# Optimization experiments

Hardware: AMD Instinct MI355X
Metric: run time of the kernel (lower is better)

The kernel has to match this reference:

```python
import jax, jax.numpy as jnp
import numpy as np

D_EMB = 256


def setup_inputs() -> dict:
    key = jax.random.key(0)
    ks = jax.random.split(key, 7)
    B, S, d = 4, 4096, D_EMB
    scale = 1.0 / np.sqrt(d)
    return {
        "x": jax.random.normal(ks[0], (B, S, d), jnp.float32),
        "Wqkv": jax.random.normal(ks[1], (d, 3 * d), jnp.float32) * scale,
        "bqkv": jax.random.normal(ks[2], (3 * d,), jnp.float32) * 0.02,
        "Wproj": jax.random.normal(ks[3], (d, d), jnp.float32) * scale,
        "bproj": jax.random.normal(ks[4], (d,), jnp.float32) * 0.02,
        "Wfc": jax.random.normal(ks[5], (d, 1), jnp.float32) * scale,
        "bfc": jax.random.normal(ks[6], (1,), jnp.float32) * 0.02,
    }


def reference(x, Wqkv, bqkv, Wproj, bproj, Wfc, bfc):
    # qkv projection: [B,S,3d] -> split into q,k,v [B,S,d]
    qkv = x @ Wqkv + bqkv
    q, k, v = jnp.split(qkv, 3, axis=2)
    # full attention scores [B,S,S]; note: original applies NO 1/sqrt(d)
    # scaling (dead branch in source), 'traditional' softmax over last dim
    attn_scores = jnp.einsum("bqd,bkd->bqk", q, k)
    attn_weights = jax.nn.softmax(attn_scores, axis=-1)
    y = jnp.einsum("bqk,bkd->bqd", attn_weights, v)
    y = y @ Wproj + bproj
    out = y @ Wfc + bfc  # [B,S,1]
    return out
```

## Files before the change

### kernel.cpp

```cpp
#include <hip/hip_runtime.h>
#include <hip/hip_bf16.h>

#define BQ 4
#define SQ 4096
#define DQ 256
#define N3 768
#define KBLK 64
#define NITER (SQ / KBLK)
#define KHALF (NITER / 2)
#define LOG2E 1.44269504f
#define THR2 11.5415603f

typedef __attribute__((ext_vector_type(8))) _Float16 f16x8;
typedef __attribute__((ext_vector_type(4))) float f32x4;
typedef __attribute__((ext_vector_type(4))) unsigned int u32x4;

__device__ __forceinline__ short f2h(float f) {
  _Float16 h = (_Float16)f;
  union { _Float16 h; short s; } v; v.h = h;
  return v.s;
}

__device__ __forceinline__ void gload16(const void* g, void* lds) {
  __builtin_amdgcn_global_load_lds(
      (const __attribute__((address_space(1))) unsigned int*)g,
      (__attribute__((address_space(3))) unsigned int*)lds, 16, 0, 0);
}

__global__ void wcomb_kernel(const float* __restrict__ Wproj,
                             const float* __restrict__ bproj,
                             const float* __restrict__ Wfc,
                             const float* __restrict__ bfc,
                             float* __restrict__ Wc) {
  __shared__ float wf[256];
  const int t = threadIdx.x;
  wf[t] = Wfc[t];
  __syncthreads();
  float acc = 0.f;
  for (int j = 0; j < 256; ++j) acc += Wproj[(size_t)t * 256 + j] * wf[j];
  Wc[t] = acc;
  if (t == 0) {
    float c = bfc[0];
    for (int j = 0; j < 256; ++j) c += bproj[j] * wf[j];
    Wc[256] = c;
  }
}

__global__ void wconv_kernel(const float* __restrict__ Wqkv,
                             short* __restrict__ W16T) {
  __shared__ float tile[64][65];
  const int nb = blockIdx.x * 64;
  const int kb = blockIdx.y * 64;
  const int t = threadIdx.x;
  const int tr = t >> 6, tc = t & 63;
#pragma unroll
  for (int i = 0; i < 16; ++i)
    tile[tr + i * 4][tc] = Wqkv[(size_t)(kb + tr + i * 4) * N3 + nb + tc];
  __syncthreads();
#pragma unroll
  for (int i = 0; i < 16; ++i)
    W16T[(size_t)(nb + tr + i * 4) * 256 + kb + tc] = f2h(tile[tc][tr + i * 4]);
}

__global__ __launch_bounds__(1024, 4) void qkv_kernel(
    const float* __restrict__ x, const short* __restrict__ W16T,
    const float* __restrict__ bqkv, const float* __restrict__ Wc,
    short* __restrict__ Qb, short* __restrict__ Kb, float* __restrict__ u) {
  __shared__ short xs[64][264];
  __shared__ short ws[2][64][256];
  __shared__ float u_red[4][4][16];
  const int t = threadIdx.x;
  const int l = t & 63, w = t >> 6;
  const int lr = l & 15, lg = l >> 4;
  const int mq = w >> 2, nq = w & 3;
  const int Mbase = blockIdx.x * 64;

#define STAGE_W(BUF, NT)                                                      \
  {                                                                           \
    _Pragma("unroll") for (int i = 0; i < 2; ++i) {                           \
      const int n = w * 4 + i * 2 + (l >> 5);                                 \
      const int gc = (l & 31) ^ (n & 7);                                      \
      gload16(W16T + (size_t)((NT)*64 + n) * 256 + gc * 8,                    \
              &ws[BUF][w * 4 + i * 2][0]);                                    \
    }                                                                         \
  }

  STAGE_W(0, 0);

  {
    const int m = t >> 4, kc = (t & 15) * 16;
    const float* src = x + (size_t)(Mbase + m) * DQ + kc;
    short tmp[16];
#pragma unroll
    for (int i = 0; i < 16; ++i) tmp[i] = f2h(src[i]);
    *(u32x4*)&xs[m][kc] = *(u32x4*)&tmp[0];
    *(u32x4*)&xs[m][kc + 8] = *(u32x4*)&tmp[8];
  }

  float bias_qk[8], bias_u[4], wc_u[4];
#pragma unroll
  for (int i = 0; i < 8; ++i) bias_qk[i] = bqkv[i * 64 + nq * 16 + lr];
#pragma unroll
  for (int i = 0; i < 4; ++i) {
    bias_u[i] = bqkv[512 + i * 64 + nq * 16 + lr];
    wc_u[i] = Wc[i * 64 + nq * 16 + lr];
  }

  __syncthreads();

  unsigned qksto[8][2];
  float upart[4] = {0.f, 0.f, 0.f, 0.f};

#pragma unroll
  for (int nt = 0; nt < 12; ++nt) {
    const int cur = nt & 1;
    if (nt + 1 < 12) {
      STAGE_W(cur ^ 1, nt + 1);
      asm volatile("s_waitcnt vmcnt(2)" ::: "memory");
    } else {
      asm volatile("s_waitcnt vmcnt(0)" ::: "memory");
    }
    __builtin_amdgcn_s_barrier();
    __builtin_amdgcn_sched_barrier(0);

    f32x4 acc = {};
    const char* wR = (const char*)&ws[cur][nq * 16 + lr][0];
#pragma unroll
    for (int kk = 0; kk < 8; ++kk) {
      f16x8 af = *(f16x8*)&xs[mq * 16 + lr][kk * 32 + lg * 8];
      f16x8 bfr = *(const f16x8*)(wR + (((4 * kk + lg) ^ (lr & 7)) << 4));
      acc = __builtin_amdgcn_mfma_f32_16x16x32_f16(af, bfr, acc, 0, 0, 0);
    }
    if (nt < 8) {
      const float sc = (nt < 4) ? 1.f : LOG2E;
      unsigned s0 = (unsigned short)f2h((acc[0] + bias_qk[nt]) * sc);
      unsigned s1 = (unsigned short)f2h((acc[1] + bias_qk[nt]) * sc);
      unsigned s2 = (unsigned short)f2h((acc[2] + bias_qk[nt]) * sc);
      unsigned s3 = (unsigned short)f2h((acc[3] + bias_qk[nt]) * sc);
      qksto[nt][0] = s0 | (s1 << 16);
      qksto[nt][1] = s2 | (s3 << 16);
    } else {
#pragma unroll
      for (int r = 0; r < 4; ++r) upart[r] += (acc[r] + bias_u[nt - 8]) * wc_u[nt - 8];
    }
    __builtin_amdgcn_s_barrier();
  }

#pragma unroll
  for (int nt = 0; nt < 8; ++nt) {
    const int col = nt * 64 + nq * 16 + lr;
#pragma unroll
    for (int r = 0; r < 4; ++r) {
      const int row = Mbase + mq * 16 + lg * 4 + r;
      const short sv = (short)((qksto[nt][r >> 1] >> ((r & 1) * 16)) & 0xFFFF);
      if (col < 256) Qb[(size_t)row * DQ + col] = sv;
      else           Kb[(size_t)row * DQ + (col - 256)] = sv;
    }
  }

#pragma unroll
  for (int mask = 1; mask <= 8; mask <<= 1)
#pragma unroll
    for (int r = 0; r < 4; ++r) upart[r] += __shfl_xor(upart[r], mask, 64);
  if (lr == 0) {
#pragma unroll
    for (int r = 0; r < 4; ++r) u_red[mq][nq][lg * 4 + r] = upart[r];
  }
  __syncthreads();
  if (t < 64)
    u[Mbase + t] = u_red[t >> 4][0][t & 15] + u_red[t >> 4][1][t & 15] +
                   u_red[t >> 4][2][t & 15] + u_red[t >> 4][3][t & 15];
#undef STAGE_W
}

__global__ __launch_bounds__(256, 2) void attn_kernel(
    const short* __restrict__ Qb, const short* __restrict__ Kb,
    const float* __restrict__ u, float* __restrict__ Pm,
    float* __restrict__ Pd, float* __restrict__ Pn) {
  __shared__ short Ks[2][64][256];
  __shared__ __align__(16) float u_lds[2048];
  __shared__ float Mrg[4][64][3];

  const int t = threadIdx.x;
  const int l = t & 63, w = t >> 6;
  const int lr = l & 15, lg = l >> 4;
  const int bid = blockIdx.x;
  const int b = bid & 3;
  const int half = (bid >> 2) & 1;
  const int qbase = (bid >> 3) * 64;

  const short* kbase = Kb + ((size_t)b * SQ + (size_t)half * (SQ / 2)) * DQ;
  const float* ubase = u + (size_t)b * SQ + half * (SQ / 2);

#define STAGE(BUF, KB)                                                      \
  {                                                                         \
    _Pragma("unroll") for (int i = 0; i < 8; ++i) {                         \
      const int kr = w * 16 + i * 2 + (l >> 5);                             \
      const int gc = (l & 31) ^ (kr & 7);                                   \
      gload16(kbase + (size_t)((KB)*64 + kr) * DQ + gc * 8,                 \
              &Ks[BUF][w * 16 + i * 2][0]);                                 \
    }                                                                       \
  }

  STAGE(0, 0);
  gload16(ubase + w * 512 + (l << 2), &u_lds[w * 512]);
  gload16(ubase + w * 512 + 256 + (l << 2), &u_lds[w * 512 + 256]);

  f16x8 qf[4][8];
#pragma unroll
  for (int mm = 0; mm < 4; ++mm) {
    const short* qptr = Qb + (size_t)(b * SQ + qbase + mm * 16 + lr) * DQ;
#pragma unroll
    for (int kk = 0; kk < 8; ++kk)
      qf[mm][kk] = *(const f16x8*)(qptr + kk * 32 + lg * 8);
  }

  float m_run[4] = {-1e30f, -1e30f, -1e30f, -1e30f};
  float num[4] = {}, den[4] = {};

  __syncthreads();

  for (int kb = 0; kb < KHALF; ++kb) {
    const int cur = kb & 1;
    if (kb + 1 < KHALF) {
      STAGE(cur ^ 1, kb + 1);
      asm volatile("s_waitcnt vmcnt(8)" ::: "memory");
    } else {
      asm volatile("s_waitcnt vmcnt(0)" ::: "memory");
    }
    __builtin_amdgcn_s_barrier();
    __builtin_amdgcn_sched_barrier(0);

    const char* kR = (const char*)&Ks[cur][w * 16 + lr][0];
    f32x4 s[4] = {};
    __builtin_amdgcn_s_setprio(1);
#pragma unroll
    for (int kk = 0; kk < 8; ++kk) {
      f16x8 kf = *(const f16x8*)(kR + (((4 * kk + lg) ^ (lr & 7)) << 4));
      s[0] = __builtin_amdgcn_mfma_f32_16x16x32_f16(kf, qf[0][kk], s[0], 0, 0, 0);
      s[1] = __builtin_amdgcn_mfma_f32_16x16x32_f16(kf, qf[1][kk], s[1], 0, 0, 0);
      s[2] = __builtin_amdgcn_mfma_f32_16x16x32_f16(kf, qf[2][kk], s[2], 0, 0, 0);
      s[3] = __builtin_amdgcn_mfma_f32_16x16x32_f16(kf, qf[3][kk], s[3], 0, 0, 0);
    }
    __builtin_amdgcn_s_setprio(0);

    bool over = false;
#pragma unroll
    for (int mm = 0; mm < 4; ++mm)
#pragma unroll
      for (int r = 0; r < 4; ++r) over = over || (s[mm][r] > m_run[mm] + THR2);
    if (__any(over)) {
#pragma unroll
      for (int mm = 0; mm < 4; ++mm) {
        float mt = fmaxf(fmaxf(s[mm][0], s[mm][1]), fmaxf(s[mm][2], s[mm][3]));
        mt = fmaxf(mt, __shfl_xor(mt, 16, 64));
        mt = fmaxf(mt, __shfl_xor(mt, 32, 64));
        const float mn = fmaxf(m_run[mm], mt);
        const float sc = exp2f(m_run[mm] - mn);
        m_run[mm] = mn;
        num[mm] *= sc;
        den[mm] *= sc;
      }
    }
    {
      const f32x4 uv = *(const f32x4*)&u_lds[kb * 64 + w * 16 + lg * 4];
#pragma unroll
      for (int mm = 0; mm < 4; ++mm)
#pragma unroll
        for (int r = 0; r < 4; ++r) {
          const float p = exp2f(s[mm][r] - m_run[mm]);
          den[mm] += p;
          num[mm] += p * uv[r];
        }
    }
    __builtin_amdgcn_s_barrier();
  }

#pragma unroll
  for (int mm = 0; mm < 4; ++mm) {
    num[mm] += __shfl_xor(num[mm], 16, 64);
    num[mm] += __shfl_xor(num[mm], 32, 64);
    den[mm] += __shfl_xor(den[mm], 16, 64);
    den[mm] += __shfl_xor(den[mm], 32, 64);
  }
  if (lg == 0) {
#pragma unroll
    for (int mm = 0; mm < 4; ++mm) {
      Mrg[w][mm * 16 + lr][0] = m_run[mm];
      Mrg[w][mm * 16 + lr][1] = den[mm];
      Mrg[w][mm * 16 + lr][2] = num[mm];
    }
  }
  __syncthreads();

  if (t < 64) {
    float M = Mrg[0][t][0];
#pragma unroll
    for (int hh = 1; hh < 4; ++hh) M = fmaxf(M, Mrg[hh][t][0]);
    float dt = 0.f, nt = 0.f;
#pragma unroll
    for (int hh = 0; hh < 4; ++hh) {
      const float e = exp2f(Mrg[hh][t][0] - M);
      dt += e * Mrg[hh][t][1];
      nt += e * Mrg[hh][t][2];
    }
    const size_t idx = (size_t)half * (BQ * SQ) + (size_t)b * SQ + qbase + t;
    Pm[idx] = M; Pd[idx] = dt; Pn[idx] = nt;
  }
#undef STAGE
}

__global__ void merge_kernel(const float* __restrict__ Pm,
                             const float* __restrict__ Pd,
                             const float* __restrict__ Pn,
                             const float* __restrict__ Wc,
                             float* __restrict__ out) {
  const int gid = blockIdx.x * 256 + threadIdx.x;
  const float m0 = Pm[gid], m1 = Pm[BQ * SQ + gid];
  const float M = fmaxf(m0, m1);
  const float e0 = exp2f(m0 - M), e1 = exp2f(m1 - M);
  const float den = e0 * Pd[gid] + e1 * Pd[BQ * SQ + gid];
  const float num = e0 * Pn[gid] + e1 * Pn[BQ * SQ + gid];
  out[gid] = num / den + Wc[256];
}

extern "C" void kernel_launch(void* const* d_in, const int* in_sizes, int n_in,
                              void* d_out, int out_size, void* d_ws, size_t ws_size,
                              hipStream_t stream) {
  const float* x     = (const float*)d_in[0];
  const float* Wqkv  = (const float*)d_in[1];
  const float* bqkv  = (const float*)d_in[2];
  const float* Wproj = (const float*)d_in[3];
  const float* bproj = (const float*)d_in[4];
  const float* Wfc   = (const float*)d_in[5];
  const float* bfc   = (const float*)d_in[6];
  float* out = (float*)d_out;

  const size_t SEG = (size_t)BQ * SQ * DQ * 2;
  char* wsb = (char*)d_ws;
  short* Qb   = (short*)(wsb);
  short* Kb   = (short*)(wsb + SEG);
  char* base  = wsb + 2 * SEG;
  float* Wc   = (float*)(base);
  float* u    = (float*)(base + 4096);
  short* W16T = (short*)(base + 4096 + 65536);
  float* Pm   = (float*)(base + 4096 + 65536 + 393216);
  float* Pd   = Pm + 2 * BQ * SQ;
  float* Pn   = Pd + 2 * BQ * SQ;

  wcomb_kernel<<<1, 256, 0, stream>>>(Wproj, bproj, Wfc, bfc, Wc);
  wconv_kernel<<<dim3(12, 4), 256, 0, stream>>>(Wqkv, W16T);
  qkv_kernel<<<256, 1024, 0, stream>>>(x, W16T, bqkv, Wc, Qb, Kb, u);
  attn_kernel<<<512, 256, 0, stream>>>(Qb, Kb, u, Pm, Pd, Pn);
  merge_kernel<<<BQ * SQ / 256, 256, 0, stream>>>(Pm, Pd, Pn, Wc, out);
}
```

Baseline: 113.9 us.

## Merge prep kernels, stage Q via LDS, restructure K pipeline, use native exp2

Fuses the weight-combine and weight-convert kernels into one launch. In the attention kernel, Q tiles are loaded through LDS with swizzled async loads instead of direct global vector loads. The K loop now issues the next stage after the barrier, with a full vmcnt(0) wait and one barrier per iteration instead of two. Other changes: swizzle offsets are precomputed, the overflow check runs on row maxima, and exp2f is replaced by the hardware exp2 builtin. The new K-loop order may expose more load latency because it waits for all outstanding loads every iteration.

After: 93.32 us. -18.1%, faster.

```diff
diff --git a/kernel.cpp b/kernel.cpp
--- a/kernel.cpp
+++ b/kernel.cpp
@@ -27,31 +27,29 @@
       (__attribute__((address_space(3))) unsigned int*)lds, 16, 0, 0);
 }
 
-__global__ void wcomb_kernel(const float* __restrict__ Wproj,
-                             const float* __restrict__ bproj,
-                             const float* __restrict__ Wfc,
-                             const float* __restrict__ bfc,
-                             float* __restrict__ Wc) {
-  __shared__ float wf[256];
+__global__ __launch_bounds__(256) void prep_kernel(
+    const float* __restrict__ Wqkv, const float* __restrict__ Wproj,
+    const float* __restrict__ bproj, const float* __restrict__ Wfc,
+    const float* __restrict__ bfc, short* __restrict__ W16T,
+    float* __restrict__ Wc) {
   const int t = threadIdx.x;
-  wf[t] = Wfc[t];
-  __syncthreads();
-  float acc = 0.f;
-  for (int j = 0; j < 256; ++j) acc += Wproj[(size_t)t * 256 + j] * wf[j];
-  Wc[t] = acc;
-  if (t == 0) {
-    float c = bfc[0];
-    for (int j = 0; j < 256; ++j) c += bproj[j] * wf[j];
-    Wc[256] = c;
-  }
-}
-
-__global__ void wconv_kernel(const float* __restrict__ Wqkv,
-                             short* __restrict__ W16T) {
+  if (blockIdx.x == 48) {
+    __shared__ float wf[256];
+    wf[t] = Wfc[t];
+    __syncthreads();
+    float acc = 0.f;
+    for (int j = 0; j < 256; ++j) acc += Wproj[(size_t)t * 256 + j] * wf[j];
+    Wc[t] = acc;
+    if (t == 0) {
+      float c = bfc[0];
+      for (int j = 0; j < 256; ++j) c += bproj[j] * wf[j];
+      Wc[256] = c;
+    }
+    return;
+  }
   __shared__ float tile[64][65];
-  const int nb = blockIdx.x * 64;
-  const int kb = blockIdx.y * 64;
-  const int t = threadIdx.x;
+  const int nb = (blockIdx.x % 12) * 64;
+  const int kb = (blockIdx.x / 12) * 64;
   const int tr = t >> 6, tc = t & 63;
 #pragma unroll
   for (int i = 0; i < 16; ++i)
@@ -202,41 +200,53 @@
     }                                                                       \
   }
 
-  STAGE(0, 0);
-  gload16(ubase + w * 512 + (l << 2), &u_lds[w * 512]);
-  gload16(ubase + w * 512 + 256 + (l << 2), &u_lds[w * 512 + 256]);
+  {
+    const short* qsrc = Qb + (size_t)(b * SQ + qbase) * DQ;
+#pragma unroll
+    for (int i = 0; i < 8; ++i) {
+      const int qr = w * 16 + i * 2 + (l >> 5);
+      const int gc = (l & 31) ^ (qr & 7);
+      gload16(qsrc + (size_t)qr * DQ + gc * 8, &Ks[0][w * 16 + i * 2][0]);
+    }
+  }
+  gload16(ubase + w * 256 + (l << 2), &u_lds[w * 256]);
+  gload16(ubase + (4 + w) * 256 + (l << 2), &u_lds[(4 + w) * 256]);
+
+  int koff[8];
+#pragma unroll
+  for (int kk = 0; kk < 8; ++kk) koff[kk] = ((4 * kk + lg) ^ (lr & 7)) << 4;
+
+  asm volatile("s_waitcnt vmcnt(0)" ::: "memory");
+  __syncthreads();
 
   f16x8 qf[4][8];
 #pragma unroll
   for (int mm = 0; mm < 4; ++mm) {
-    const short* qptr = Qb + (size_t)(b * SQ + qbase + mm * 16 + lr) * DQ;
+    const char* qR = (const char*)&Ks[0][mm * 16 + lr][0];
 #pragma unroll
     for (int kk = 0; kk < 8; ++kk)
-      qf[mm][kk] = *(const f16x8*)(qptr + kk * 32 + lg * 8);
-  }
+      qf[mm][kk] = *(const f16x8*)(qR + koff[kk]);
+  }
+  __syncthreads();
 
   float m_run[4] = {-1e30f, -1e30f, -1e30f, -1e30f};
   float num[4] = {}, den[4] = {};
 
-  __syncthreads();
+  STAGE(0, 0);
 
   for (int kb = 0; kb < KHALF; ++kb) {
     const int cur = kb & 1;
-    if (kb + 1 < KHALF) {
-      STAGE(cur ^ 1, kb + 1);
-      asm volatile("s_waitcnt vmcnt(8)" ::: "memory");
-    } else {
-      asm volatile("s_waitcnt vmcnt(0)" ::: "memory");
-    }
+    asm volatile("s_waitcnt vmcnt(0)" ::: "memory");
     __builtin_amdgcn_s_barrier();
     __builtin_amdgcn_sched_barrier(0);
+    if (kb + 1 < KHALF) STAGE(cur ^ 1, kb + 1);
 
     const char* kR = (const char*)&Ks[cur][w * 16 + lr][0];
     f32x4 s[4] = {};
     __builtin_amdgcn_s_setprio(1);
 #pragma unroll
     for (int kk = 0; kk < 8; ++kk) {
-      f16x8 kf = *(const f16x8*)(kR + (((4 * kk + lg) ^ (lr & 7)) << 4));
+      f16x8 kf = *(const f16x8*)(kR + koff[kk]);
       s[0] = __builtin_amdgcn_mfma_f32_16x16x32_f16(kf, qf[0][kk], s[0], 0, 0, 0);
       s[1] = __builtin_amdgcn_mfma_f32_16x16x32_f16(kf, qf[1][kk], s[1], 0, 0, 0);
       s[2] = __builtin_amdgcn_mfma_f32_16x16x32_f16(kf, qf[2][kk], s[2], 0, 0, 0);
@@ -244,19 +254,20 @@
     }
     __builtin_amdgcn_s_setprio(0);
 
-    bool over = false;
+    float mx[4];
 #pragma unroll
     for (int mm = 0; mm < 4; ++mm)
-#pragma unroll
-      for (int r = 0; r < 4; ++r) over = over || (s[mm][r] > m_run[mm] + THR2);
+      mx[mm] = fmaxf(fmaxf(s[mm][0], s[mm][1]), fmaxf(s[mm][2], s[mm][3]));
+    const bool over = (mx[0] > m_run[0] + THR2) || (mx[1] > m_run[1] + THR2) ||
+                      (mx[2] > m_run[2] + THR2) || (mx[3] > m_run[3] + THR2);
     if (__any(over)) {
 #pragma unroll
       for (int mm = 0; mm < 4; ++mm) {
-        float mt = fmaxf(fmaxf(s[mm][0], s[mm][1]), fmaxf(s[mm][2], s[mm][3]));
+        float mt = mx[mm];
         mt = fmaxf(mt, __shfl_xor(mt, 16, 64));
         mt = fmaxf(mt, __shfl_xor(mt, 32, 64));
         const float mn = fmaxf(m_run[mm], mt);
-        const float sc = exp2f(m_run[mm] - mn);
+        const float sc = __builtin_amdgcn_exp2f(m_run[mm] - mn);
         m_run[mm] = mn;
         num[mm] *= sc;
         den[mm] *= sc;
@@ -268,12 +279,11 @@
       for (int mm = 0; mm < 4; ++mm)
 #pragma unroll
         for (int r = 0; r < 4; ++r) {
-          const float p = exp2f(s[mm][r] - m_run[mm]);
+          const float p = __builtin_amdgcn_exp2f(s[mm][r] - m_run[mm]);
           den[mm] += p;
           num[mm] += p * uv[r];
         }
     }
-    __builtin_amdgcn_s_barrier();
   }
 
 #pragma unroll
@@ -300,7 +310,7 @@
     float dt = 0.f, nt = 0.f;
 #pragma unroll
     for (int hh = 0; hh < 4; ++hh) {
-      const float e = exp2f(Mrg[hh][t][0] - M);
+      const float e = __builtin_amdgcn_exp2f(Mrg[hh][t][0] - M);
       dt += e * Mrg[hh][t][1];
       nt += e * Mrg[hh][t][2];
     }
@@ -318,7 +328,8 @@
   const int gid = blockIdx.x * 256 + threadIdx.x;
   const float m0 = Pm[gid], m1 = Pm[BQ * SQ + gid];
   const float M = fmaxf(m0, m1);
-  const float e0 = exp2f(m0 - M), e1 = exp2f(m1 - M);
+  const float e0 = __builtin_amdgcn_exp2f(m0 - M);
+  const float e1 = __builtin_amdgcn_exp2f(m1 - M);
   const float den = e0 * Pd[gid] + e1 * Pd[BQ * SQ + gid];
   const float num = e0 * Pn[gid] + e1 * Pn[BQ * SQ + gid];
   out[gid] = num / den + Wc[256];
@@ -348,8 +359,7 @@
   float* Pd   = Pm + 2 * BQ * SQ;
   float* Pn   = Pd + 2 * BQ * SQ;
 
-  wcomb_kernel<<<1, 256, 0, stream>>>(Wproj, bproj, Wfc, bfc, Wc);
-  wconv_kernel<<<dim3(12, 4), 256, 0, stream>>>(Wqkv, W16T);
+  prep_kernel<<<49, 256, 0, stream>>>(Wqkv, Wproj, bproj, Wfc, bfc, W16T, Wc);
   qkv_kernel<<<256, 1024, 0, stream>>>(x, W16T, bqkv, Wc, Qb, Kb, u);
   attn_kernel<<<512, 256, 0, stream>>>(Qb, Kb, u, Pm, Pd, Pn);
   merge_kernel<<<BQ * SQ / 256, 256, 0, stream>>>(Pm, Pd, Pn, Wc, out);
```
